# Performance work log

Measured on AMD Instinct MI355X. Metric: run time of the kernel, lower is better.

The kernel has to match this reference:

```python
import jax, jax.numpy as jnp
import numpy as np

D = 64
H = 8


def setup_inputs() -> dict:
    key = jax.random.key(0)
    ks = jax.random.split(key, 6)
    b, l = 2, 4096
    scale = 1.0 / np.sqrt(D)
    x = jax.random.normal(ks[0], (b, l, D), dtype=jnp.float32)
    Wq = jax.random.normal(ks[1], (D, D * H), dtype=jnp.float32) * scale
    Wk = jax.random.normal(ks[2], (D, D * H), dtype=jnp.float32) * scale
    Wv = jax.random.normal(ks[3], (D, D * H), dtype=jnp.float32) * scale
    Wu = jax.random.normal(ks[4], (H * D, D), dtype=jnp.float32) * (1.0 / np.sqrt(H * D))
    bu = jax.random.normal(ks[5], (D,), dtype=jnp.float32) * 0.01
    return {"x": x, "Wq": Wq, "Wk": Wk, "Wv": Wv, "Wu": Wu, "bu": bu}


def reference(x, Wq, Wk, Wv, Wu, bu):
    b, l, d = x.shape
    h = H
    # per-head projections: each head uses FULL width d (as in the torch module)
    q = jnp.einsum('bld,de->ble', x, Wq).reshape(b, l, h, d)
    k = jnp.einsum('bld,de->ble', x, Wk).reshape(b, l, h, d)
    v = jnp.einsum('bld,de->ble', x, Wv).reshape(b, l, h, d)
    # scores [b,h,l,l] scaled by 1/sqrt(d)
    scores = jnp.einsum('blhd,bmhd->bhlm', q, k) / jnp.sqrt(jnp.asarray(d, x.dtype))
    w = jax.nn.softmax(scores, axis=-1)
    out = jnp.einsum('bhlm,bmhd->blhd', w, v).reshape(b, l, h * d)
    return out @ Wu + bu
```

## Files before the change

kernel.cpp:

```cpp
#include <hip/hip_runtime.h>
#include <hip/hip_bf16.h>
#include <stdint.h>

typedef float    f32x16 __attribute__((ext_vector_type(16)));
typedef float    f32x4  __attribute__((ext_vector_type(4)));
typedef __bf16   bf16x8 __attribute__((ext_vector_type(8)));
typedef uint32_t u32x4  __attribute__((ext_vector_type(4)));

#define WS_QG    0
#define WS_KG    8388608
#define WS_VTG   16777216
#define WS_ATTN  25165824
#define WS_WT    33554432
#define WS_WUT   33751040

__device__ __forceinline__ f32x16 zero16(){
  f32x16 z;
  #pragma unroll
  for (int i = 0; i < 16; ++i) z[i] = 0.0f;
  return z;
}

__device__ __forceinline__ uint16_t bf16b(float v){
  return __builtin_bit_cast(uint16_t, __float2bfloat16(v));
}

__device__ __forceinline__ uint32_t pk2(float a, float b){
  return (uint32_t)bf16b(a) | ((uint32_t)bf16b(b) << 16);
}

__device__ __forceinline__ void plswap(uint32_t &a, uint32_t &b){
  asm volatile("v_permlane32_swap_b32 %0, %1" : "+v"(a), "+v"(b));
}

__device__ __forceinline__ float sum16(const f32x16& s){
  float a0 = (s[0]+s[1]) + (s[2]+s[3]),   a1 = (s[4]+s[5]) + (s[6]+s[7]);
  float a2 = (s[8]+s[9]) + (s[10]+s[11]), a3 = (s[12]+s[13]) + (s[14]+s[15]);
  return (a0 + a1) + (a2 + a3);
}

__device__ __forceinline__ void bar_ws(){
  asm volatile("s_waitcnt lgkmcnt(0)" ::: "memory");
  __builtin_amdgcn_s_barrier();
  asm volatile("" ::: "memory");
}

__global__ void prep_w(const float* __restrict__ Wq, const float* __restrict__ Wk,
                       const float* __restrict__ Wv, const float* __restrict__ Wu,
                       char* __restrict__ ws){
  int tid = blockIdx.x * 256 + threadIdx.x;
  if (tid < 3*32768){
    int which = tid >> 15;
    int idx   = tid & 32767;
    int e = idx & 511, k = idx >> 9;
    const float* W = (which == 0) ? Wq : (which == 1 ? Wk : Wv);
    float v = W[k*512 + e];
    if (which == 0) v *= 0.18033688011112042f;
    ((uint16_t*)(ws + WS_WT))[which*32768 + e*64 + k] = bf16b(v);
  } else {
    int idx = tid - 3*32768;
    int c = idx & 63, e = idx >> 6;
    ((uint16_t*)(ws + WS_WUT))[c*512 + e] = bf16b(Wu[e*64 + c]);
  }
}

__global__ __launch_bounds__(256,2) void qkv_proj(const float* __restrict__ x,
                                                  char* __restrict__ ws){
  const int lane = threadIdx.x & 63;
  const int widx = threadIdx.x >> 6;
  const int x8 = blockIdx.x & 7;
  const int o  = blockIdx.x >> 3;
  const int rt = x8*32 + o/6;
  const int rem = (o%6)*4 + widx;
  const int mm = rem >> 3, cb = rem & 7;
  const int col  = lane & 31, hi = lane >> 5;

  __shared__ __align__(16) uint16_t tbuf[4][2560];

  const uint16_t* Wt = (const uint16_t*)(ws + WS_WT) + mm*32768;

  bf16x8 af[4];
  {
    const float* xr = x + (size_t)(rt*32 + col)*64 + hi*8;
    #pragma unroll
    for (int ks = 0; ks < 4; ++ks){
      float4 a0 = *(const float4*)(xr + ks*16);
      float4 a1 = *(const float4*)(xr + ks*16 + 4);
      uint4 u;
      u.x = pk2(a0.x, a0.y); u.y = pk2(a0.z, a0.w);
      u.z = pk2(a1.x, a1.y); u.w = pk2(a1.z, a1.w);
      af[ks] = __builtin_bit_cast(bf16x8, u);
    }
  }

  f32x16 acc0 = zero16(), acc1 = zero16();
  {
    const uint16_t* w0p = Wt + (size_t)(cb*64 + col)*64 + hi*8;
    const uint16_t* w1p = w0p + 32*64;
    #pragma unroll
    for (int ks = 0; ks < 4; ++ks){
      bf16x8 b0 = *(const bf16x8*)(w0p + ks*16);
      bf16x8 b1 = *(const bf16x8*)(w1p + ks*16);
      acc0 = __builtin_amdgcn_mfma_f32_32x32x16_bf16(af[ks], b0, acc0, 0, 0, 0);
      acc1 = __builtin_amdgcn_mfma_f32_32x32x16_bf16(af[ks], b1, acc1, 0, 0, 0);
    }
  }

  uint16_t* Qg  = (uint16_t*)(ws + WS_QG);
  uint16_t* Kg  = (uint16_t*)(ws + WS_KG);
  uint16_t* Vtg = (uint16_t*)(ws + WS_VTG);
  uint16_t* tb  = tbuf[widx];
  const int b     = (rt*32) >> 12;
  const int ltok0 = (rt*32) & 4095;
  if (mm == 2){
    #pragma unroll
    for (int r = 0; r < 16; ++r){
      int tok = (r&3) + 8*(r>>2) + 4*hi;
      tb[col*40 + tok]        = bf16b(acc0[r]);
      tb[(col+32)*40 + tok]   = bf16b(acc1[r]);
    }
    const int vrow = lane >> 2, ch = lane & 3;
    #pragma unroll
    for (int o2 = 0; o2 < 4; ++o2){
      int dv = o2*16 + vrow;
      u32x4 u = *(const u32x4*)(tb + dv*40 + ch*8);
      *(u32x4*)(Vtg + ((size_t)((b*8 + cb)*64 + dv))*4096 + ltok0 + ch*8) = u;
    }
  } else {
    uint16_t* G = mm ? Kg : Qg;
    #pragma unroll
    for (int r = 0; r < 16; ++r){
      int tok = (r&3) + 8*(r>>2) + 4*hi;
      tb[tok*72 + col]      = bf16b(acc0[r]);
      tb[tok*72 + 32 + col] = bf16b(acc1[r]);
    }
    const int rr2 = lane >> 3, ch2 = lane & 7;
    size_t base = (size_t)((b*8 + cb)*4096 + ltok0)*64;
    #pragma unroll
    for (int o2 = 0; o2 < 4; ++o2){
      int tok = o2*8 + rr2;
      u32x4 uu = *(const u32x4*)(tb + tok*72 + ch2*8);
      *(u32x4*)(G + base + (size_t)tok*64 + ch2*8) = uu;
    }
  }
}

__global__ __launch_bounds__(256,2) void attn_fa(char* __restrict__ ws){
  const int lane = threadIdx.x & 63;
  const int wave = threadIdx.x >> 6;
  const int qh = wave & 1, kvh = wave >> 1;
  const int u   = blockIdx.x >> 3;
  const int bh  = (blockIdx.x & 7) + ((u >> 5) << 3);
  const int qt  = u & 31;
  const int col = lane & 31, hi = lane >> 5;
  const int kxor = (col & 7) << 4;

  const uint16_t* Qg  = (const uint16_t*)(ws + WS_QG)  + (size_t)bh*262144;
  const uint16_t* Kg  = (const uint16_t*)(ws + WS_KG)  + (size_t)bh*262144;
  const uint16_t* Vtg = (const uint16_t*)(ws + WS_VTG) + (size_t)bh*262144;
  uint16_t* attn = (uint16_t*)(ws + WS_ATTN);

  __shared__ __align__(16) char smem[65536];
  char* sbase = smem + kvh*32768;
  char* buf0 = sbase;
  char* buf1 = sbase + 16384;

  const int qbase = qt*128 + qh*64;

  bf16x8 qf0[4], qf1[4];
  {
    const uint16_t* qr0 = Qg + (size_t)(qbase + col)*64 + hi*8;
    const uint16_t* qr1 = qr0 + 32*64;
    #pragma unroll
    for (int ds = 0; ds < 4; ++ds){
      qf0[ds] = *(const bf16x8*)(qr0 + ds*16);
      qf1[ds] = *(const bf16x8*)(qr1 + ds*16);
    }
  }

  const int rr = lane >> 3, ch = lane & 7;
  const int srow = qh*8 + rr;
  const uint16_t* kSrcB = Kg  + (size_t)(kvh*2048 + srow)*64 + ch*8;
  const uint16_t* vSrcB = Vtg + (size_t)srow*4096 + kvh*2048 + ch*8;
  const int sDstB = srow*128 + ((ch*16) ^ (rr << 4));

  f32x16 ot00 = zero16(), ot01 = zero16(), ot10 = zero16(), ot11 = zero16();
  float rs0 = 0.0f, rs1 = 0.0f;

  u32x4 rK[4], rV[4];
  auto loadKV = [&](int t){
    const uint16_t* ks = kSrcB + (size_t)t*4096;
    const uint16_t* vs = vSrcB + t*64;
    #pragma unroll
    for (int o2 = 0; o2 < 4; ++o2) rK[o2] = *(const u32x4*)(ks + o2*1024);
    #pragma unroll
    for (int o2 = 0; o2 < 4; ++o2) rV[o2] = *(const u32x4*)(vs + (size_t)o2*65536);
  };
  auto writeKV = [&](char* buf){
    #pragma unroll
    for (int o2 = 0; o2 < 4; ++o2) *(u32x4*)(buf + sDstB + o2*2048) = rK[o2];
    #pragma unroll
    for (int o2 = 0; o2 < 4; ++o2) *(u32x4*)(buf + 8192 + sDstB + o2*2048) = rV[o2];
  };

  auto pack2 = [&](const f32x16& s, bf16x8& f0, bf16x8& f1){
    uint32_t w0 = pk2(s[0],  s[1]),  w1 = pk2(s[2],  s[3]);
    uint32_t w2 = pk2(s[4],  s[5]),  w3 = pk2(s[6],  s[7]);
    uint32_t w4 = pk2(s[8],  s[9]),  w5 = pk2(s[10], s[11]);
    uint32_t w6 = pk2(s[12], s[13]), w7 = pk2(s[14], s[15]);
    plswap(w0, w2); plswap(w1, w3); plswap(w4, w6); plswap(w5, w7);
    u32x4 u0; u0.x = w0; u0.y = w1; u0.z = w2; u0.w = w3;
    u32x4 u1; u1.x = w4; u1.y = w5; u1.z = w6; u1.w = w7;
    f0 = __builtin_bit_cast(bf16x8, u0);
    f1 = __builtin_bit_cast(bf16x8, u1);
  };

  auto compute = [&](const char* buf){
    const char* kb = buf;
    const char* vb = buf + 8192;
    bf16x8 pA[4], pB[4];
    #pragma unroll
    for (int ks2 = 0; ks2 < 2; ++ks2){
      f32x16 sA = zero16(), sB = zero16();
      __builtin_amdgcn_s_setprio(1);
      #pragma unroll
      for (int ds = 0; ds < 4; ++ds){
        bf16x8 kf = *(const bf16x8*)(kb + (ks2*32 + col)*128 + ((ds*32 + hi*16) ^ kxor));
        sA = __builtin_amdgcn_mfma_f32_32x32x16_bf16(kf, qf0[ds], sA, 0, 0, 0);
        sB = __builtin_amdgcn_mfma_f32_32x32x16_bf16(kf, qf1[ds], sB, 0, 0, 0);
      }
      __builtin_amdgcn_s_setprio(0);
      #pragma unroll
      for (int r = 0; r < 16; ++r) sA[r] = __builtin_amdgcn_exp2f(sA[r]);
      #pragma unroll
      for (int r = 0; r < 16; ++r) sB[r] = __builtin_amdgcn_exp2f(sB[r]);
      rs0 += sum16(sA);
      rs1 += sum16(sB);
      pack2(sA, pA[ks2*2], pA[ks2*2+1]);
      pack2(sB, pB[ks2*2], pB[ks2*2+1]);
    }
    __builtin_amdgcn_s_setprio(1);
    #pragma unroll
    for (int sl = 0; sl < 4; ++sl){
      bf16x8 vf0 = *(const bf16x8*)(vb + col*128 + ((sl*32 + hi*16) ^ kxor));
      ot00 = __builtin_amdgcn_mfma_f32_32x32x16_bf16(vf0, pA[sl], ot00, 0, 0, 0);
      ot01 = __builtin_amdgcn_mfma_f32_32x32x16_bf16(vf0, pB[sl], ot01, 0, 0, 0);
      bf16x8 vf1 = *(const bf16x8*)(vb + (32 + col)*128 + ((sl*32 + hi*16) ^ kxor));
      ot10 = __builtin_amdgcn_mfma_f32_32x32x16_bf16(vf1, pA[sl], ot10, 0, 0, 0);
      ot11 = __builtin_amdgcn_mfma_f32_32x32x16_bf16(vf1, pB[sl], ot11, 0, 0, 0);
    }
    __builtin_amdgcn_s_setprio(0);
  };

  loadKV(0);
  writeKV(buf0);
  loadKV(1);
  bar_ws();

  for (int t = 0; t < 32; ++t){
    char* cur = (t & 1) ? buf1 : buf0;
    char* nxt = (t & 1) ? buf0 : buf1;
    writeKV(nxt);
    loadKV((t+2 < 32) ? t+2 : 31);
    compute(cur);
    bar_ws();
  }

  float* m = (float*)(smem + qh*17408) + lane*68;
  if (kvh){
    #pragma unroll
    for (int j = 0; j < 4; ++j){
      *(f32x4*)(m +      4*j) = f32x4{ot00[4*j], ot00[4*j+1], ot00[4*j+2], ot00[4*j+3]};
      *(f32x4*)(m + 16 + 4*j) = f32x4{ot01[4*j], ot01[4*j+1], ot01[4*j+2], ot01[4*j+3]};
      *(f32x4*)(m + 32 + 4*j) = f32x4{ot10[4*j], ot10[4*j+1], ot10[4*j+2], ot10[4*j+3]};
      *(f32x4*)(m + 48 + 4*j) = f32x4{ot11[4*j], ot11[4*j+1], ot11[4*j+2], ot11[4*j+3]};
    }
    m[64] = rs0; m[65] = rs1;
  }
  bar_ws();
  if (!kvh){
    #pragma unroll
    for (int j = 0; j < 4; ++j){
      f32x4 v0 = *(const f32x4*)(m +      4*j);
      f32x4 v1 = *(const f32x4*)(m + 16 + 4*j);
      f32x4 v2 = *(const f32x4*)(m + 32 + 4*j);
      f32x4 v3 = *(const f32x4*)(m + 48 + 4*j);
      #pragma unroll
      for (int e = 0; e < 4; ++e){
        ot00[4*j+e] += v0[e]; ot01[4*j+e] += v1[e];
        ot10[4*j+e] += v2[e]; ot11[4*j+e] += v3[e];
      }
    }
    rs0 += m[64];  rs1 += m[65];
    rs0 += __shfl_xor(rs0, 32);
    rs1 += __shfl_xor(rs1, 32);
    float inv0 = 1.0f / rs0, inv1 = 1.0f / rs1;

    uint32_t* ow = (uint32_t*)(smem + 36864 + qh*8448);
    #pragma unroll
    for (int od = 0; od < 2; ++od){
      #pragma unroll
      for (int j = 0; j < 8; ++j){
        int p = (j&1) + 4*(j>>1) + 2*hi + 16*od;
        const f32x16& a0 = od ? ot10 : ot00;
        const f32x16& a1 = od ? ot11 : ot01;
        ow[(col     )*33 + p] = pk2(a0[2*j]*inv0, a0[2*j+1]*inv0);
        ow[(col + 32)*33 + p] = pk2(a1[2*j]*inv1, a1[2*j+1]*inv1);
      }
    }
    const int rrE = lane >> 3, chE = lane & 7;
    #pragma unroll
    for (int oo = 0; oo < 8; ++oo){
      int q = oo*8 + rrE;
      u32x4 uu = *(const u32x4*)(ow + q*33 + chE*4);
      size_t row = (size_t)((bh >> 3)*4096 + qbase + q);
      *(u32x4*)(attn + row*512 + (bh & 7)*64 + chE*8) = uu;
    }
  }
}

__global__ __launch_bounds__(256) void out_proj(const char* __restrict__ ws,
                                                const float* __restrict__ bu,
                                                float* __restrict__ out){
  const int lane = threadIdx.x & 63;
  const int wave = blockIdx.x*4 + (threadIdx.x >> 6);
  const int mt = wave >> 2, cb = wave & 3;
  const int rc = lane & 15, kg = lane >> 4;

  const uint16_t* attn = (const uint16_t*)(ws + WS_ATTN);
  const uint16_t* Wut  = (const uint16_t*)(ws + WS_WUT);

  const uint16_t* ar = attn + (size_t)(mt*16 + rc)*512 + kg*8;
  const uint16_t* bp = Wut  + (size_t)(cb*16 + rc)*512 + kg*8;

  f32x4 acc = {0.0f, 0.0f, 0.0f, 0.0f};
  #pragma unroll
  for (int ks = 0; ks < 16; ++ks){
    bf16x8 af = *(const bf16x8*)(ar + ks*32);
    bf16x8 bf = *(const bf16x8*)(bp + ks*32);
    acc = __builtin_amdgcn_mfma_f32_16x16x32_bf16(af, bf, acc, 0, 0, 0);
  }
  float bias = bu[cb*16 + rc];
  #pragma unroll
  for (int r = 0; r < 4; ++r){
    int orow = mt*16 + kg*4 + r;
    out[(size_t)orow*64 + cb*16 + rc] = acc[r] + bias;
  }
}

extern "C" void kernel_launch(void* const* d_in, const int* in_sizes, int n_in,
                              void* d_out, int out_size, void* d_ws, size_t ws_size,
                              hipStream_t stream){
  const float* x  = (const float*)d_in[0];
  const float* Wq = (const float*)d_in[1];
  const float* Wk = (const float*)d_in[2];
  const float* Wv = (const float*)d_in[3];
  const float* Wu = (const float*)d_in[4];
  const float* bu = (const float*)d_in[5];
  char*  ws  = (char*)d_ws;
  float* out = (float*)d_out;

  prep_w  <<<dim3(512),  dim3(256), 0, stream>>>(Wq, Wk, Wv, Wu, ws);
  qkv_proj<<<dim3(1536), dim3(256), 0, stream>>>(x, ws);
  attn_fa <<<dim3(512),  dim3(256), 0, stream>>>(ws);
  out_proj<<<dim3(512),  dim3(256), 0, stream>>>(ws, bu, out);
}
```

Baseline: 178.9 us.

## Restructure attention with direct global-to-LDS loads, 4-way KV split, repacked weights

The attention kernel now gives each block 64 queries and splits the KV range across four waves. K/V tiles are staged with global_load_lds directly into a single small per-wave LDS buffer, replacing the register round-trip double buffer, and the four partial results are combined through a staged LDS tree reduction. The P matrix is packed with the hardware v_cvt_pk_bf16_f32 instruction, and occupancy is raised to 3 blocks per CU. The QKV projection has each wave compute three tiles over a pre-swizzled weight layout written by prep_w, cutting the grid to a third; the risk is lost overlap from single buffering and the extra reduction barriers.

After: 184.6 us. 3.2% more time.

```diff
diff --git a/kernel.cpp b/kernel.cpp
--- a/kernel.cpp
+++ b/kernel.cpp
@@ -29,6 +29,12 @@
   return (uint32_t)bf16b(a) | ((uint32_t)bf16b(b) << 16);
 }
 
+__device__ __forceinline__ uint32_t cvtpk(float a, float b){
+  uint32_t r;
+  asm("v_cvt_pk_bf16_f32 %0, %1, %2" : "=v"(r) : "v"(a), "v"(b));
+  return r;
+}
+
 __device__ __forceinline__ void plswap(uint32_t &a, uint32_t &b){
   asm volatile("v_permlane32_swap_b32 %0, %1" : "+v"(a), "+v"(b));
 }
@@ -39,6 +45,12 @@
   return (a0 + a1) + (a2 + a3);
 }
 
+__device__ __forceinline__ void gl16(const uint16_t* g, char* l){
+  __builtin_amdgcn_global_load_lds(
+      (const __attribute__((address_space(1))) uint32_t*)g,
+      (__attribute__((address_space(3))) uint32_t*)l, 16, 0, 0);
+}
+
 __device__ __forceinline__ void bar_ws(){
   asm volatile("s_waitcnt lgkmcnt(0)" ::: "memory");
   __builtin_amdgcn_s_barrier();
@@ -49,16 +61,22 @@
                        const float* __restrict__ Wv, const float* __restrict__ Wu,
                        char* __restrict__ ws){
   int tid = blockIdx.x * 256 + threadIdx.x;
-  if (tid < 3*32768){
-    int which = tid >> 15;
-    int idx   = tid & 32767;
-    int e = idx & 511, k = idx >> 9;
-    const float* W = (which == 0) ? Wq : (which == 1 ? Wk : Wv);
+  if (tid < 98304){
+    int j  = tid & 7;
+    int ln = (tid >> 3) & 63;
+    int hf = (tid >> 9) & 1;
+    int ks = (tid >> 10) & 3;
+    int cb = (tid >> 12) & 7;
+    int mm = tid >> 15;
+    int colW = ln & 31, hiW = ln >> 5;
+    int k = ks*16 + hiW*8 + j;
+    int e = cb*64 + colW + 32*hf;
+    const float* W = (mm == 0) ? Wq : (mm == 1 ? Wk : Wv);
     float v = W[k*512 + e];
-    if (which == 0) v *= 0.18033688011112042f;
-    ((uint16_t*)(ws + WS_WT))[which*32768 + e*64 + k] = bf16b(v);
+    if (mm == 0) v *= 0.18033688011112042f;
+    ((uint16_t*)(ws + WS_WT))[tid] = bf16b(v);
   } else {
-    int idx = tid - 3*32768;
+    int idx = tid - 98304;
     int c = idx & 63, e = idx >> 6;
     ((uint16_t*)(ws + WS_WUT))[c*512 + e] = bf16b(Wu[e*64 + c]);
   }
@@ -70,14 +88,13 @@
   const int widx = threadIdx.x >> 6;
   const int x8 = blockIdx.x & 7;
   const int o  = blockIdx.x >> 3;
-  const int rt = x8*32 + o/6;
-  const int rem = (o%6)*4 + widx;
-  const int mm = rem >> 3, cb = rem & 7;
+  const int rt   = x8*32 + (o >> 1);
+  const int half = o & 1;
   const int col  = lane & 31, hi = lane >> 5;
 
   __shared__ __align__(16) uint16_t tbuf[4][2560];
 
-  const uint16_t* Wt = (const uint16_t*)(ws + WS_WT) + mm*32768;
+  const uint16_t* Wf = (const uint16_t*)(ws + WS_WT);
 
   bf16x8 af[4];
   {
@@ -93,84 +110,89 @@
     }
   }
 
-  f32x16 acc0 = zero16(), acc1 = zero16();
-  {
-    const uint16_t* w0p = Wt + (size_t)(cb*64 + col)*64 + hi*8;
-    const uint16_t* w1p = w0p + 32*64;
-    #pragma unroll
-    for (int ks = 0; ks < 4; ++ks){
-      bf16x8 b0 = *(const bf16x8*)(w0p + ks*16);
-      bf16x8 b1 = *(const bf16x8*)(w1p + ks*16);
-      acc0 = __builtin_amdgcn_mfma_f32_32x32x16_bf16(af[ks], b0, acc0, 0, 0, 0);
-      acc1 = __builtin_amdgcn_mfma_f32_32x32x16_bf16(af[ks], b1, acc1, 0, 0, 0);
-    }
-  }
-
   uint16_t* Qg  = (uint16_t*)(ws + WS_QG);
   uint16_t* Kg  = (uint16_t*)(ws + WS_KG);
   uint16_t* Vtg = (uint16_t*)(ws + WS_VTG);
   uint16_t* tb  = tbuf[widx];
   const int b     = (rt*32) >> 12;
   const int ltok0 = (rt*32) & 4095;
-  if (mm == 2){
-    #pragma unroll
-    for (int r = 0; r < 16; ++r){
-      int tok = (r&3) + 8*(r>>2) + 4*hi;
-      tb[col*40 + tok]        = bf16b(acc0[r]);
-      tb[(col+32)*40 + tok]   = bf16b(acc1[r]);
-    }
-    const int vrow = lane >> 2, ch = lane & 3;
-    #pragma unroll
-    for (int o2 = 0; o2 < 4; ++o2){
-      int dv = o2*16 + vrow;
-      u32x4 u = *(const u32x4*)(tb + dv*40 + ch*8);
-      *(u32x4*)(Vtg + ((size_t)((b*8 + cb)*64 + dv))*4096 + ltok0 + ch*8) = u;
-    }
-  } else {
-    uint16_t* G = mm ? Kg : Qg;
-    #pragma unroll
-    for (int r = 0; r < 16; ++r){
-      int tok = (r&3) + 8*(r>>2) + 4*hi;
-      tb[tok*72 + col]      = bf16b(acc0[r]);
-      tb[tok*72 + 32 + col] = bf16b(acc1[r]);
-    }
-    const int rr2 = lane >> 3, ch2 = lane & 7;
-    size_t base = (size_t)((b*8 + cb)*4096 + ltok0)*64;
-    #pragma unroll
-    for (int o2 = 0; o2 < 4; ++o2){
-      int tok = o2*8 + rr2;
-      u32x4 uu = *(const u32x4*)(tb + tok*72 + ch2*8);
-      *(u32x4*)(G + base + (size_t)tok*64 + ch2*8) = uu;
-    }
-  }
-}
-
-__global__ __launch_bounds__(256,2) void attn_fa(char* __restrict__ ws){
+
+  #pragma unroll
+  for (int ti = 0; ti < 3; ++ti){
+    const int rem = half*12 + widx*3 + ti;
+    const int mm = rem >> 3, cb = rem & 7;
+
+    f32x16 acc0 = zero16(), acc1 = zero16();
+    {
+      const uint16_t* wp = Wf + (size_t)((mm*8 + cb)*4)*1024 + lane*8;
+      #pragma unroll
+      for (int ks = 0; ks < 4; ++ks){
+        bf16x8 b0 = *(const bf16x8*)(wp + ks*1024);
+        bf16x8 b1 = *(const bf16x8*)(wp + ks*1024 + 512);
+        acc0 = __builtin_amdgcn_mfma_f32_32x32x16_bf16(af[ks], b0, acc0, 0, 0, 0);
+        acc1 = __builtin_amdgcn_mfma_f32_32x32x16_bf16(af[ks], b1, acc1, 0, 0, 0);
+      }
+    }
+
+    if (mm == 2){
+      #pragma unroll
+      for (int r = 0; r < 16; ++r){
+        int tok = (r&3) + 8*(r>>2) + 4*hi;
+        tb[col*40 + tok]        = bf16b(acc0[r]);
+        tb[(col+32)*40 + tok]   = bf16b(acc1[r]);
+      }
+      const int vrow = lane >> 2, ch = lane & 3;
+      #pragma unroll
+      for (int o2 = 0; o2 < 4; ++o2){
+        int dv = o2*16 + vrow;
+        u32x4 u = *(const u32x4*)(tb + dv*40 + ch*8);
+        *(u32x4*)(Vtg + ((size_t)((b*8 + cb)*64 + dv))*4096 + ltok0 + ch*8) = u;
+      }
+    } else {
+      uint16_t* G = mm ? Kg : Qg;
+      #pragma unroll
+      for (int r = 0; r < 16; ++r){
+        int tok = (r&3) + 8*(r>>2) + 4*hi;
+        tb[tok*72 + col]      = bf16b(acc0[r]);
+        tb[tok*72 + 32 + col] = bf16b(acc1[r]);
+      }
+      const int rr2 = lane >> 3, ch2 = lane & 7;
+      size_t base = (size_t)((b*8 + cb)*4096 + ltok0)*64;
+      #pragma unroll
+      for (int o2 = 0; o2 < 4; ++o2){
+        int tok = o2*8 + rr2;
+        u32x4 uu = *(const u32x4*)(tb + tok*72 + ch2*8);
+        *(u32x4*)(G + base + (size_t)tok*64 + ch2*8) = uu;
+      }
+    }
+  }
+}
+
+__global__ __launch_bounds__(256,3) void attn_fa(char* __restrict__ ws){
   const int lane = threadIdx.x & 63;
-  const int wave = threadIdx.x >> 6;
-  const int qh = wave & 1, kvh = wave >> 1;
-  const int u   = blockIdx.x >> 3;
-  const int bh  = (blockIdx.x & 7) + ((u >> 5) << 3);
-  const int qt  = u & 31;
+  const int kvh  = threadIdx.x >> 6;
+  const int u    = blockIdx.x >> 3;
+  const int bh   = (blockIdx.x & 7) + ((u >> 6) << 3);
+  const int qt   = u & 63;
   const int col = lane & 31, hi = lane >> 5;
   const int kxor = (col & 7) << 4;
+  const int vxor = (col & 3) << 4;
 
   const uint16_t* Qg  = (const uint16_t*)(ws + WS_QG)  + (size_t)bh*262144;
   const uint16_t* Kg  = (const uint16_t*)(ws + WS_KG)  + (size_t)bh*262144;
   const uint16_t* Vtg = (const uint16_t*)(ws + WS_VTG) + (size_t)bh*262144;
   uint16_t* attn = (uint16_t*)(ws + WS_ATTN);
 
-  __shared__ __align__(16) char smem[65536];
-  char* sbase = smem + kvh*32768;
-  char* buf0 = sbase;
-  char* buf1 = sbase + 16384;
-
-  const int qbase = qt*128 + qh*64;
+  __shared__ __align__(16) char smem[36864];
+  char* kb = smem + kvh*9216;
+  char* vb = kb + 4096;
+
+  const int qbase = qt*64;
 
   bf16x8 qf0[4], qf1[4];
   {
     const uint16_t* qr0 = Qg + (size_t)(qbase + col)*64 + hi*8;
-    const uint16_t* qr1 = qr0 + 32*64;
+    const uint16_t* qr1 = qr0 + 2048;
     #pragma unroll
     for (int ds = 0; ds < 4; ++ds){
       qf0[ds] = *(const bf16x8*)(qr0 + ds*16);
@@ -179,142 +201,163 @@
   }
 
   const int rr = lane >> 3, ch = lane & 7;
-  const int srow = qh*8 + rr;
-  const uint16_t* kSrcB = Kg  + (size_t)(kvh*2048 + srow)*64 + ch*8;
-  const uint16_t* vSrcB = Vtg + (size_t)srow*4096 + kvh*2048 + ch*8;
-  const int sDstB = srow*128 + ((ch*16) ^ (rr << 4));
+  const int vr = lane >> 2, c4 = lane & 3;
+  const uint16_t* kS = Kg  + (size_t)(kvh*1024 + rr)*64 + (ch ^ rr)*8;
+  const uint16_t* vS = Vtg + (size_t)vr*4096 + kvh*1024 + (c4 ^ (vr & 3))*8;
 
   f32x16 ot00 = zero16(), ot01 = zero16(), ot10 = zero16(), ot11 = zero16();
   float rs0 = 0.0f, rs1 = 0.0f;
 
-  u32x4 rK[4], rV[4];
-  auto loadKV = [&](int t){
-    const uint16_t* ks = kSrcB + (size_t)t*4096;
-    const uint16_t* vs = vSrcB + t*64;
-    #pragma unroll
-    for (int o2 = 0; o2 < 4; ++o2) rK[o2] = *(const u32x4*)(ks + o2*1024);
-    #pragma unroll
-    for (int o2 = 0; o2 < 4; ++o2) rV[o2] = *(const u32x4*)(vs + (size_t)o2*65536);
-  };
-  auto writeKV = [&](char* buf){
-    #pragma unroll
-    for (int o2 = 0; o2 < 4; ++o2) *(u32x4*)(buf + sDstB + o2*2048) = rK[o2];
-    #pragma unroll
-    for (int o2 = 0; o2 < 4; ++o2) *(u32x4*)(buf + 8192 + sDstB + o2*2048) = rV[o2];
-  };
-
-  auto pack2 = [&](const f32x16& s, bf16x8& f0, bf16x8& f1){
-    uint32_t w0 = pk2(s[0],  s[1]),  w1 = pk2(s[2],  s[3]);
-    uint32_t w2 = pk2(s[4],  s[5]),  w3 = pk2(s[6],  s[7]);
-    uint32_t w4 = pk2(s[8],  s[9]),  w5 = pk2(s[10], s[11]);
-    uint32_t w6 = pk2(s[12], s[13]), w7 = pk2(s[14], s[15]);
-    plswap(w0, w2); plswap(w1, w3); plswap(w4, w6); plswap(w5, w7);
-    u32x4 u0; u0.x = w0; u0.y = w1; u0.z = w2; u0.w = w3;
-    u32x4 u1; u1.x = w4; u1.y = w5; u1.z = w6; u1.w = w7;
-    f0 = __builtin_bit_cast(bf16x8, u0);
-    f1 = __builtin_bit_cast(bf16x8, u1);
-  };
-
-  auto compute = [&](const char* buf){
-    const char* kb = buf;
-    const char* vb = buf + 8192;
-    bf16x8 pA[4], pB[4];
-    #pragma unroll
-    for (int ks2 = 0; ks2 < 2; ++ks2){
-      f32x16 sA = zero16(), sB = zero16();
-      __builtin_amdgcn_s_setprio(1);
-      #pragma unroll
-      for (int ds = 0; ds < 4; ++ds){
-        bf16x8 kf = *(const bf16x8*)(kb + (ks2*32 + col)*128 + ((ds*32 + hi*16) ^ kxor));
-        sA = __builtin_amdgcn_mfma_f32_32x32x16_bf16(kf, qf0[ds], sA, 0, 0, 0);
-        sB = __builtin_amdgcn_mfma_f32_32x32x16_bf16(kf, qf1[ds], sB, 0, 0, 0);
-      }
-      __builtin_amdgcn_s_setprio(0);
-      #pragma unroll
-      for (int r = 0; r < 16; ++r) sA[r] = __builtin_amdgcn_exp2f(sA[r]);
-      #pragma unroll
-      for (int r = 0; r < 16; ++r) sB[r] = __builtin_amdgcn_exp2f(sB[r]);
-      rs0 += sum16(sA);
-      rs1 += sum16(sB);
-      pack2(sA, pA[ks2*2], pA[ks2*2+1]);
-      pack2(sB, pB[ks2*2], pB[ks2*2+1]);
-    }
+  #define STAGE(T){                                                   \
+    const uint16_t* k_ = kS + (size_t)(T)*2048;                       \
+    gl16(k_,        kb);        gl16(k_ + 512,  kb + 1024);           \
+    gl16(k_ + 1024, kb + 2048); gl16(k_ + 1536, kb + 3072);           \
+    const uint16_t* v_ = vS + (T)*32;                                 \
+    gl16(v_,          vb);        gl16(v_ + 65536,  vb + 1024);       \
+    gl16(v_ + 131072, vb + 2048); gl16(v_ + 196608, vb + 3072); }
+
+  STAGE(0);
+
+  #pragma unroll 1
+  for (int t = 0; t < 32; ++t){
+    asm volatile("s_waitcnt vmcnt(0)" ::: "memory");
+
+    f32x16 sA = zero16(), sB = zero16();
     __builtin_amdgcn_s_setprio(1);
     #pragma unroll
-    for (int sl = 0; sl < 4; ++sl){
-      bf16x8 vf0 = *(const bf16x8*)(vb + col*128 + ((sl*32 + hi*16) ^ kxor));
-      ot00 = __builtin_amdgcn_mfma_f32_32x32x16_bf16(vf0, pA[sl], ot00, 0, 0, 0);
-      ot01 = __builtin_amdgcn_mfma_f32_32x32x16_bf16(vf0, pB[sl], ot01, 0, 0, 0);
-      bf16x8 vf1 = *(const bf16x8*)(vb + (32 + col)*128 + ((sl*32 + hi*16) ^ kxor));
-      ot10 = __builtin_amdgcn_mfma_f32_32x32x16_bf16(vf1, pA[sl], ot10, 0, 0, 0);
-      ot11 = __builtin_amdgcn_mfma_f32_32x32x16_bf16(vf1, pB[sl], ot11, 0, 0, 0);
+    for (int ds = 0; ds < 4; ++ds){
+      bf16x8 kf = *(const bf16x8*)(kb + col*128 + ((ds*32 + hi*16) ^ kxor));
+      sA = __builtin_amdgcn_mfma_f32_32x32x16_bf16(kf, qf0[ds], sA, 0, 0, 0);
+      sB = __builtin_amdgcn_mfma_f32_32x32x16_bf16(kf, qf1[ds], sB, 0, 0, 0);
     }
     __builtin_amdgcn_s_setprio(0);
-  };
-
-  loadKV(0);
-  writeKV(buf0);
-  loadKV(1);
-  bar_ws();
-
-  for (int t = 0; t < 32; ++t){
-    char* cur = (t & 1) ? buf1 : buf0;
-    char* nxt = (t & 1) ? buf0 : buf1;
-    writeKV(nxt);
-    loadKV((t+2 < 32) ? t+2 : 31);
-    compute(cur);
+
+    #pragma unroll
+    for (int r = 0; r < 16; ++r) sA[r] = __builtin_amdgcn_exp2f(sA[r]);
+    #pragma unroll
+    for (int r = 0; r < 16; ++r) sB[r] = __builtin_amdgcn_exp2f(sB[r]);
+    rs0 += sum16(sA);
+    rs1 += sum16(sB);
+
+    bf16x8 pA0, pA1, pB0, pB1;
+    {
+      uint32_t w0 = cvtpk(sA[0],  sA[1]),  w1 = cvtpk(sA[2],  sA[3]);
+      uint32_t w2 = cvtpk(sA[4],  sA[5]),  w3 = cvtpk(sA[6],  sA[7]);
+      uint32_t w4 = cvtpk(sA[8],  sA[9]),  w5 = cvtpk(sA[10], sA[11]);
+      uint32_t w6 = cvtpk(sA[12], sA[13]), w7 = cvtpk(sA[14], sA[15]);
+      plswap(w0, w2); plswap(w1, w3); plswap(w4, w6); plswap(w5, w7);
+      u32x4 u0; u0.x = w0; u0.y = w1; u0.z = w2; u0.w = w3;
+      u32x4 u1; u1.x = w4; u1.y = w5; u1.z = w6; u1.w = w7;
+      pA0 = __builtin_bit_cast(bf16x8, u0);
+      pA1 = __builtin_bit_cast(bf16x8, u1);
+      uint32_t y0 = cvtpk(sB[0],  sB[1]),  y1 = cvtpk(sB[2],  sB[3]);
+      uint32_t y2 = cvtpk(sB[4],  sB[5]),  y3 = cvtpk(sB[6],  sB[7]);
+      uint32_t y4 = cvtpk(sB[8],  sB[9]),  y5 = cvtpk(sB[10], sB[11]);
+      uint32_t y6 = cvtpk(sB[12], sB[13]), y7 = cvtpk(sB[14], sB[15]);
+      plswap(y0, y2); plswap(y1, y3); plswap(y4, y6); plswap(y5, y7);
+      u32x4 u2; u2.x = y0; u2.y = y1; u2.z = y2; u2.w = y3;
+      u32x4 u3; u3.x = y4; u3.y = y5; u3.z = y6; u3.w = y7;
+      pB0 = __builtin_bit_cast(bf16x8, u2);
+      pB1 = __builtin_bit_cast(bf16x8, u3);
+    }
+
+    __builtin_amdgcn_s_setprio(1);
+    #pragma unroll
+    for (int ks = 0; ks < 2; ++ks){
+      bf16x8 pa = ks ? pA1 : pA0;
+      bf16x8 pb = ks ? pB1 : pB0;
+      bf16x8 v0 = *(const bf16x8*)(vb + col*64 + ((ks*32 + hi*16) ^ vxor));
+      ot00 = __builtin_amdgcn_mfma_f32_32x32x16_bf16(v0, pa, ot00, 0, 0, 0);
+      ot01 = __builtin_amdgcn_mfma_f32_32x32x16_bf16(v0, pb, ot01, 0, 0, 0);
+      bf16x8 v1 = *(const bf16x8*)(vb + (col+32)*64 + ((ks*32 + hi*16) ^ vxor));
+      ot10 = __builtin_amdgcn_mfma_f32_32x32x16_bf16(v1, pa, ot10, 0, 0, 0);
+      ot11 = __builtin_amdgcn_mfma_f32_32x32x16_bf16(v1, pb, ot11, 0, 0, 0);
+    }
+    __builtin_amdgcn_s_setprio(0);
+
+    asm volatile("s_waitcnt lgkmcnt(0)" ::: "memory");
+    if (t < 31) STAGE(t+1);
+  }
+  #undef STAGE
+
+  {
+    float* mOwn = (float*)(smem + kvh*9216) + lane*34;
+    float* mUp  = (float*)(smem + ((kvh < 3 ? kvh+1 : 3))*9216) + lane*34;
+    float* mR2  = (float*)(smem + 2*9216) + lane*34;
+    float* mR3  = (float*)(smem + 3*9216) + lane*34;
+
+    auto dumpH0 = [&](float* m){
+      #pragma unroll
+      for (int j = 0; j < 4; ++j){
+        *(f32x4*)(m +      4*j) = f32x4{ot00[4*j], ot00[4*j+1], ot00[4*j+2], ot00[4*j+3]};
+        *(f32x4*)(m + 16 + 4*j) = f32x4{ot01[4*j], ot01[4*j+1], ot01[4*j+2], ot01[4*j+3]};
+      }
+      m[32] = rs0; m[33] = rs1;
+    };
+    auto dumpH1 = [&](float* m){
+      #pragma unroll
+      for (int j = 0; j < 4; ++j){
+        *(f32x4*)(m +      4*j) = f32x4{ot10[4*j], ot10[4*j+1], ot10[4*j+2], ot10[4*j+3]};
+        *(f32x4*)(m + 16 + 4*j) = f32x4{ot11[4*j], ot11[4*j+1], ot11[4*j+2], ot11[4*j+3]};
+      }
+    };
+    auto addH0 = [&](const float* m){
+      #pragma unroll
+      for (int j = 0; j < 4; ++j){
+        f32x4 a = *(const f32x4*)(m + 4*j);
+        f32x4 b = *(const f32x4*)(m + 16 + 4*j);
+        #pragma unroll
+        for (int e = 0; e < 4; ++e){ ot00[4*j+e] += a[e]; ot01[4*j+e] += b[e]; }
+      }
+      rs0 += m[32]; rs1 += m[33];
+    };
+    auto addH1 = [&](const float* m){
+      #pragma unroll
+      for (int j = 0; j < 4; ++j){
+        f32x4 a = *(const f32x4*)(m + 4*j);
+        f32x4 b = *(const f32x4*)(m + 16 + 4*j);
+        #pragma unroll
+        for (int e = 0; e < 4; ++e){ ot10[4*j+e] += a[e]; ot11[4*j+e] += b[e]; }
+      }
+    };
+
+    if (kvh & 1) dumpH0(mOwn);
     bar_ws();
-  }
-
-  float* m = (float*)(smem + qh*17408) + lane*68;
-  if (kvh){
-    #pragma unroll
-    for (int j = 0; j < 4; ++j){
-      *(f32x4*)(m +      4*j) = f32x4{ot00[4*j], ot00[4*j+1], ot00[4*j+2], ot00[4*j+3]};
-      *(f32x4*)(m + 16 + 4*j) = f32x4{ot01[4*j], ot01[4*j+1], ot01[4*j+2], ot01[4*j+3]};
-      *(f32x4*)(m + 32 + 4*j) = f32x4{ot10[4*j], ot10[4*j+1], ot10[4*j+2], ot10[4*j+3]};
-      *(f32x4*)(m + 48 + 4*j) = f32x4{ot11[4*j], ot11[4*j+1], ot11[4*j+2], ot11[4*j+3]};
-    }
-    m[64] = rs0; m[65] = rs1;
-  }
-  bar_ws();
-  if (!kvh){
-    #pragma unroll
-    for (int j = 0; j < 4; ++j){
-      f32x4 v0 = *(const f32x4*)(m +      4*j);
-      f32x4 v1 = *(const f32x4*)(m + 16 + 4*j);
-      f32x4 v2 = *(const f32x4*)(m + 32 + 4*j);
-      f32x4 v3 = *(const f32x4*)(m + 48 + 4*j);
-      #pragma unroll
-      for (int e = 0; e < 4; ++e){
-        ot00[4*j+e] += v0[e]; ot01[4*j+e] += v1[e];
-        ot10[4*j+e] += v2[e]; ot11[4*j+e] += v3[e];
-      }
-    }
-    rs0 += m[64];  rs1 += m[65];
-    rs0 += __shfl_xor(rs0, 32);
-    rs1 += __shfl_xor(rs1, 32);
-    float inv0 = 1.0f / rs0, inv1 = 1.0f / rs1;
-
-    uint32_t* ow = (uint32_t*)(smem + 36864 + qh*8448);
-    #pragma unroll
-    for (int od = 0; od < 2; ++od){
-      #pragma unroll
-      for (int j = 0; j < 8; ++j){
-        int p = (j&1) + 4*(j>>1) + 2*hi + 16*od;
-        const f32x16& a0 = od ? ot10 : ot00;
-        const f32x16& a1 = od ? ot11 : ot01;
-        ow[(col     )*33 + p] = pk2(a0[2*j]*inv0, a0[2*j+1]*inv0);
-        ow[(col + 32)*33 + p] = pk2(a1[2*j]*inv1, a1[2*j+1]*inv1);
-      }
-    }
-    const int rrE = lane >> 3, chE = lane & 7;
-    #pragma unroll
-    for (int oo = 0; oo < 8; ++oo){
-      int q = oo*8 + rrE;
-      u32x4 uu = *(const u32x4*)(ow + q*33 + chE*4);
-      size_t row = (size_t)((bh >> 3)*4096 + qbase + q);
-      *(u32x4*)(attn + row*512 + (bh & 7)*64 + chE*8) = uu;
+    if (!(kvh & 1)) addH0(mUp);
+    bar_ws();
+    if (kvh & 1) dumpH1(mOwn);
+    bar_ws();
+    if (!(kvh & 1)) addH1(mUp);
+    bar_ws();
+    if (kvh == 2){ dumpH0(mOwn); dumpH1(mR3); }
+    bar_ws();
+    if (kvh == 0){
+      addH0(mR2); addH1(mR3);
+
+      rs0 += __shfl_xor(rs0, 32);
+      rs1 += __shfl_xor(rs1, 32);
+      float inv0 = 1.0f / rs0, inv1 = 1.0f / rs1;
+
+      uint32_t* ow = (uint32_t*)smem;
+      #pragma unroll
+      for (int od = 0; od < 2; ++od){
+        #pragma unroll
+        for (int j = 0; j < 8; ++j){
+          int p = (j&1) + 4*(j>>1) + 2*hi + 16*od;
+          const f32x16& a0 = od ? ot10 : ot00;
+          const f32x16& a1 = od ? ot11 : ot01;
+          ow[col*33 + p]      = pk2(a0[2*j]*inv0, a0[2*j+1]*inv0);
+          ow[(col+32)*33 + p] = pk2(a1[2*j]*inv1, a1[2*j+1]*inv1);
+        }
+      }
+      const int rrE = lane >> 3, chE = lane & 7;
+      #pragma unroll
+      for (int oo = 0; oo < 8; ++oo){
+        int q = oo*8 + rrE;
+        u32x4 uu = *(const u32x4*)(ow + q*33 + chE*4);
+        size_t row = (size_t)((bh >> 3)*4096 + qbase + q);
+        *(u32x4*)(attn + row*512 + (bh & 7)*64 + chE*8) = uu;
+      }
     }
   }
 }
@@ -361,7 +404,7 @@
   float* out = (float*)d_out;
 
   prep_w  <<<dim3(512),  dim3(256), 0, stream>>>(Wq, Wk, Wv, Wu, ws);
-  qkv_proj<<<dim3(1536), dim3(256), 0, stream>>>(x, ws);
-  attn_fa <<<dim3(512),  dim3(256), 0, stream>>>(ws);
+  qkv_proj<<<dim3(512),  dim3(256), 0, stream>>>(x, ws);
+  attn_fa <<<dim3(1024), dim3(256), 0, stream>>>(ws);
   out_proj<<<dim3(512),  dim3(256), 0, stream>>>(ws, bu, out);
 }
```
